# Optimization experiments

Measured on AMD Instinct MI355X. Metric: run time of the kernel, lower is better.

## Reference

```python
import jax, jax.numpy as jnp
import numpy as np
from jax import lax


def setup_inputs() -> dict:
    key = jax.random.key(0)
    k1, k2, k3 = jax.random.split(key, 3)
    B, D_IN, D_OUT, DEPTH = 16384, 768, 768, 11
    n_nodes = 2 ** (DEPTH + 1) - 1  # 4095
    l1 = 1.0 / np.sqrt(D_IN)
    l2 = 1.0 / np.sqrt(n_nodes)
    x = jax.random.normal(k1, (B, D_IN), dtype=jnp.float32)
    w1s = jax.random.uniform(k2, (D_IN * n_nodes, 1), minval=-l1, maxval=l1, dtype=jnp.float32)
    w2s = jax.random.uniform(k3, (n_nodes, D_OUT), minval=-l2, maxval=l2, dtype=jnp.float32)
    return {"x": x, "w1s": w1s, "w2s": w2s, "depth": DEPTH}


def reference(x, w1s, w2s, depth):
    # x: [B, d_in]; w1s: [d_in * n_nodes, 1]; w2s: [n_nodes, d_out]
    B, d_in = x.shape
    n_nodes = w2s.shape[0]
    W1 = w1s.reshape(n_nodes, d_in)  # per-node routing hyperplanes

    def step(nodes, _):
        # logit[b] = <x[b], W1[nodes[b]]>  (the per-sample selected-row dot)
        logits = jnp.einsum('bd,bd->b', x, W1[nodes])
        next_nodes = nodes * 2 + (logits >= 0).astype(nodes.dtype) + 1
        return next_nodes, (nodes, logits)

    init = jnp.zeros((B,), dtype=jnp.int32)
    _, (all_nodes, all_logits) = lax.scan(step, init, None, length=depth + 1)
    all_nodes = all_nodes.T                      # [B, depth+1]
    acts = jax.nn.gelu(all_logits.T, approximate=False)  # torch F.gelu is exact erf
    # out[b] = sum_i acts[b,i] * w2s[all_nodes[b,i]]
    out = jnp.einsum('bk,bko->bo', acts, w2s[all_nodes])
    return out
```

## Files before the change

### kernel.cpp

```cpp
#include <hip/hip_runtime.h>
#include <math.h>


#define FFF_LVLS 12
#define FFF_D 768
#define FFF_ROWF4 192
#define FFF_NODES 4095
#define WAVES_PER_BLOCK 16

typedef unsigned short u16x8 __attribute__((ext_vector_type(8)));
typedef unsigned short u16x4 __attribute__((ext_vector_type(4)));

__device__ __forceinline__ float gelu_exact(float v) {
    return 0.5f * v * (1.0f + erff(v * 0.70710678118654752440f));
}

__device__ __forceinline__ unsigned short f32_to_bf16_rne(float f) {
    unsigned int u = __builtin_bit_cast(unsigned int, f);
    u += 0x7FFFu + ((u >> 16) & 1u);
    return (unsigned short)(u >> 16);
}
__device__ __forceinline__ float bf(unsigned short h) {
    return __builtin_bit_cast(float, (unsigned int)h << 16);
}

template <int CTRL>
__device__ __forceinline__ float dpp_shr_add(float v) {
    const int t = __builtin_amdgcn_update_dpp(
        0, __builtin_bit_cast(int, v), CTRL, 0xf, 0xf, true);
    return v + __builtin_bit_cast(float, t);
}

__device__ __forceinline__ float wave_allsum_f32(float v) {
    v = dpp_shr_add<0x111>(v);
    v = dpp_shr_add<0x112>(v);
    v = dpp_shr_add<0x114>(v);
    v = dpp_shr_add<0x118>(v);
    const int i15 = __builtin_amdgcn_readlane(__builtin_bit_cast(int, v), 15);
    const int i31 = __builtin_amdgcn_readlane(__builtin_bit_cast(int, v), 31);
    const int i47 = __builtin_amdgcn_readlane(__builtin_bit_cast(int, v), 47);
    const int i63 = __builtin_amdgcn_readlane(__builtin_bit_cast(int, v), 63);
    return (__builtin_bit_cast(float, i15) + __builtin_bit_cast(float, i31))
         + (__builtin_bit_cast(float, i47) + __builtin_bit_cast(float, i63));
}

__global__ void __launch_bounds__(1024) fff_convert_kernel(
    const float4* __restrict__ w1, const float4* __restrict__ w2,
    ushort4* __restrict__ o1, ushort4* __restrict__ o2, int nf4)
{
    int i = blockIdx.x * blockDim.x + threadIdx.x;
    if (i < nf4) {
        const float4 v = w1[i];
        ushort4 h;
        h.x = f32_to_bf16_rne(v.x); h.y = f32_to_bf16_rne(v.y);
        h.z = f32_to_bf16_rne(v.z); h.w = f32_to_bf16_rne(v.w);
        o1[i] = h;
    } else if (i < 2 * nf4) {
        const int j = i - nf4;
        const float4 v = w2[j];
        ushort4 h;
        h.x = f32_to_bf16_rne(v.x); h.y = f32_to_bf16_rne(v.y);
        h.z = f32_to_bf16_rne(v.z); h.w = f32_to_bf16_rne(v.w);
        o2[j] = h;
    }
}

__global__ void __launch_bounds__(1024) fff_sparse_kernel_bf16(
    const float* __restrict__ x,
    const float* __restrict__ w1s,
    const unsigned short* __restrict__ w1b,
    const unsigned short* __restrict__ w2b,
    float* __restrict__ out,
    int B)
{
    const int wave = threadIdx.x >> 6;
    const int lane = threadIdx.x & 63;
    const int b = blockIdx.x * WAVES_PER_BLOCK + wave;
    if (b >= B) return;

    const float4* __restrict__ xf4 = (const float4*)(x) + (size_t)b * FFF_ROWF4;

    const float4 xA0 = xf4[2 * lane];
    const float4 xA1 = xf4[2 * lane + 1];
    const float4 xB  = xf4[128 + lane];

    float acts[FFF_LVLS];
    int bits = 0;
    int node = 0;

#pragma unroll
    for (int lvl = 0; lvl < FFF_LVLS; ++lvl) {
        const unsigned short* __restrict__ row = w1b + (size_t)node * FFF_D;
        const u16x8 hA = ((const u16x8*)row)[lane];
        const u16x4 hB = ((const u16x4*)(row + 512))[lane];

        float q0 = xA0.x * bf(hA[0]);
        float q1 = xA0.y * bf(hA[1]);
        q0 = fmaf(xA0.z, bf(hA[2]), q0);
        q1 = fmaf(xA0.w, bf(hA[3]), q1);
        q0 = fmaf(xA1.x, bf(hA[4]), q0);
        q1 = fmaf(xA1.y, bf(hA[5]), q1);
        q0 = fmaf(xA1.z, bf(hA[6]), q0);
        q1 = fmaf(xA1.w, bf(hA[7]), q1);
        q0 = fmaf(xB.x,  bf(hB[0]), q0);
        q1 = fmaf(xB.y,  bf(hB[1]), q1);
        q0 = fmaf(xB.z,  bf(hB[2]), q0);
        q1 = fmaf(xB.w,  bf(hB[3]), q1);

        float p = wave_allsum_f32(q0 + q1);

        if (__builtin_expect(fabsf(p) < 0.03f, 0)) {
            const float4* __restrict__ rf = (const float4*)w1s
                                          + (size_t)node * FFF_ROWF4;
            const float4 a0 = rf[2 * lane];
            const float4 a1 = rf[2 * lane + 1];
            const float4 a2 = rf[128 + lane];
            double d0 = (double)xA0.x * (double)a0.x;
            double d1 = (double)xA0.y * (double)a0.y;
            d0 += (double)xA0.z * (double)a0.z;
            d1 += (double)xA0.w * (double)a0.w;
            d0 += (double)xA1.x * (double)a1.x;
            d1 += (double)xA1.y * (double)a1.y;
            d0 += (double)xA1.z * (double)a1.z;
            d1 += (double)xA1.w * (double)a1.w;
            d0 += (double)xB.x  * (double)a2.x;
            d1 += (double)xB.y  * (double)a2.y;
            d0 += (double)xB.z  * (double)a2.z;
            d1 += (double)xB.w  * (double)a2.w;
            double pd = d0 + d1;
#pragma unroll
            for (int m = 32; m > 0; m >>= 1) pd += __shfl_xor(pd, m, 64);
            p = (float)pd;
        }

        acts[lvl] = gelu_exact(p);
        const int s = (p >= 0.0f) ? 1 : 0;
        bits |= s << lvl;
        node = 2 * node + 1 + s;
    }

    float4 accA0 = make_float4(0.f, 0.f, 0.f, 0.f);
    float4 accA1 = make_float4(0.f, 0.f, 0.f, 0.f);
    float4 accB  = make_float4(0.f, 0.f, 0.f, 0.f);

    node = 0;
#pragma unroll
    for (int lvl = 0; lvl < FFF_LVLS; ++lvl) {
        const unsigned short* __restrict__ row = w2b + (size_t)node * FFF_D;
        const u16x8 hA = ((const u16x8*)row)[lane];
        const u16x4 hB = ((const u16x4*)(row + 512))[lane];
        const float a = acts[lvl];
        accA0.x = fmaf(a, bf(hA[0]), accA0.x);
        accA0.y = fmaf(a, bf(hA[1]), accA0.y);
        accA0.z = fmaf(a, bf(hA[2]), accA0.z);
        accA0.w = fmaf(a, bf(hA[3]), accA0.w);
        accA1.x = fmaf(a, bf(hA[4]), accA1.x);
        accA1.y = fmaf(a, bf(hA[5]), accA1.y);
        accA1.z = fmaf(a, bf(hA[6]), accA1.z);
        accA1.w = fmaf(a, bf(hA[7]), accA1.w);
        accB.x  = fmaf(a, bf(hB[0]), accB.x);
        accB.y  = fmaf(a, bf(hB[1]), accB.y);
        accB.z  = fmaf(a, bf(hB[2]), accB.z);
        accB.w  = fmaf(a, bf(hB[3]), accB.w);
        node = 2 * node + 1 + ((bits >> lvl) & 1);
    }

    float4* __restrict__ of4 = (float4*)(out) + (size_t)b * FFF_ROWF4;
    of4[2 * lane]     = accA0;
    of4[2 * lane + 1] = accA1;
    of4[128 + lane]   = accB;
}

__global__ void __launch_bounds__(1024) fff_sparse_kernel_f32(
    const float* __restrict__ x,
    const float* __restrict__ w1s,
    const float* __restrict__ w2s,
    float* __restrict__ out,
    int B)
{
    const int wave = threadIdx.x >> 6;
    const int lane = threadIdx.x & 63;
    const int b = blockIdx.x * WAVES_PER_BLOCK + wave;
    if (b >= B) return;

    const float4* __restrict__ xf4  = (const float4*)x;
    const float4* __restrict__ w1f4 = (const float4*)w1s;
    const float4* __restrict__ w2f4 = (const float4*)w2s;

    const int xb = b * FFF_ROWF4 + lane;
    const float4 xv0 = xf4[xb];
    const float4 xv1 = xf4[xb + 64];
    const float4 xv2 = xf4[xb + 128];

    float acts[FFF_LVLS];
    int bits = 0;
    int node = 0;

#pragma unroll
    for (int lvl = 0; lvl < FFF_LVLS; ++lvl) {
        const int r = node * FFF_ROWF4 + lane;
        const float4 a0 = w1f4[r];
        const float4 a1 = w1f4[r + 64];
        const float4 a2 = w1f4[r + 128];
        float q0 = xv0.x * a0.x;
        float q1 = xv0.y * a0.y;
        q0 = fmaf(xv0.z, a0.z, q0);
        q1 = fmaf(xv0.w, a0.w, q1);
        q0 = fmaf(xv1.x, a1.x, q0);
        q1 = fmaf(xv1.y, a1.y, q1);
        q0 = fmaf(xv1.z, a1.z, q0);
        q1 = fmaf(xv1.w, a1.w, q1);
        q0 = fmaf(xv2.x, a2.x, q0);
        q1 = fmaf(xv2.y, a2.y, q1);
        q0 = fmaf(xv2.z, a2.z, q0);
        q1 = fmaf(xv2.w, a2.w, q1);
        float p = wave_allsum_f32(q0 + q1);
        if (__builtin_expect(fabsf(p) < 1e-4f, 0)) {
            double d0 = (double)xv0.x * (double)a0.x;
            double d1 = (double)xv0.y * (double)a0.y;
            d0 += (double)xv0.z * (double)a0.z;
            d1 += (double)xv0.w * (double)a0.w;
            d0 += (double)xv1.x * (double)a1.x;
            d1 += (double)xv1.y * (double)a1.y;
            d0 += (double)xv1.z * (double)a1.z;
            d1 += (double)xv1.w * (double)a1.w;
            d0 += (double)xv2.x * (double)a2.x;
            d1 += (double)xv2.y * (double)a2.y;
            d0 += (double)xv2.z * (double)a2.z;
            d1 += (double)xv2.w * (double)a2.w;
            double pd = d0 + d1;
#pragma unroll
            for (int m = 32; m > 0; m >>= 1) pd += __shfl_xor(pd, m, 64);
            p = (float)pd;
        }
        acts[lvl] = gelu_exact(p);
        const int s = (p >= 0.0f) ? 1 : 0;
        bits |= s << lvl;
        node = 2 * node + 1 + s;
    }

    float4 acc0 = make_float4(0.f, 0.f, 0.f, 0.f);
    float4 acc1 = make_float4(0.f, 0.f, 0.f, 0.f);
    float4 acc2 = make_float4(0.f, 0.f, 0.f, 0.f);
    node = 0;
#pragma unroll
    for (int lvl = 0; lvl < FFF_LVLS; ++lvl) {
        const int r = node * FFF_ROWF4 + lane;
        const float4 c0 = w2f4[r];
        const float4 c1 = w2f4[r + 64];
        const float4 c2 = w2f4[r + 128];
        const float a = acts[lvl];
        acc0.x = fmaf(a, c0.x, acc0.x); acc0.y = fmaf(a, c0.y, acc0.y);
        acc0.z = fmaf(a, c0.z, acc0.z); acc0.w = fmaf(a, c0.w, acc0.w);
        acc1.x = fmaf(a, c1.x, acc1.x); acc1.y = fmaf(a, c1.y, acc1.y);
        acc1.z = fmaf(a, c1.z, acc1.z); acc1.w = fmaf(a, c1.w, acc1.w);
        acc2.x = fmaf(a, c2.x, acc2.x); acc2.y = fmaf(a, c2.y, acc2.y);
        acc2.z = fmaf(a, c2.z, acc2.z); acc2.w = fmaf(a, c2.w, acc2.w);
        node = 2 * node + 1 + ((bits >> lvl) & 1);
    }

    float4* __restrict__ of4 = (float4*)out;
    const int ob = b * FFF_ROWF4 + lane;
    of4[ob]       = acc0;
    of4[ob + 64]  = acc1;
    of4[ob + 128] = acc2;
}

extern "C" void kernel_launch(void* const* d_in, const int* in_sizes, int n_in,
                              void* d_out, int out_size, void* d_ws, size_t ws_size,
                              hipStream_t stream) {
    const float* x   = (const float*)d_in[0];
    const float* w1s = (const float*)d_in[1];
    const float* w2s = (const float*)d_in[2];
    float* out = (float*)d_out;

    const int B = out_size / FFF_D;
    const int blocks = (B + WAVES_PER_BLOCK - 1) / WAVES_PER_BLOCK;

    const size_t n_elems = (size_t)FFF_NODES * FFF_D;
    const size_t needed = 2 * n_elems * sizeof(unsigned short);

    if (ws_size >= needed) {
        unsigned short* w1b = (unsigned short*)d_ws;
        unsigned short* w2b = w1b + n_elems;
        const int nf4 = (int)(n_elems / 4);
        const int cblocks = (2 * nf4 + 1023) / 1024;
        fff_convert_kernel<<<cblocks, 1024, 0, stream>>>(
            (const float4*)w1s, (const float4*)w2s,
            (ushort4*)w1b, (ushort4*)w2b, nf4);
        fff_sparse_kernel_bf16<<<blocks, WAVES_PER_BLOCK * 64, 0, stream>>>(
            x, w1s, w1b, w2b, out, B);
    } else {
        fff_sparse_kernel_f32<<<blocks, WAVES_PER_BLOCK * 64, 0, stream>>>(
            x, w1s, w2s, out, B);
    }
}
```

Before: 66.40 us.

## Fuse routing and output accumulation into one loop with overlapped row loads

Merges the tree-routing loop and the output accumulation loop into a single pass. At each level the W2 row for the current node and the W1 row for the next node are both issued right after the branch decision, so the W2 gather and GELU/FMA work overlap the latency of the next W1 load. This removes the stored acts/bits and the second serial chain of dependent loads, at the cost of more live registers in the unrolled loop.

```diff
diff --git a/kernel.cpp b/kernel.cpp
--- a/kernel.cpp
+++ b/kernel.cpp
@@ -84,28 +84,29 @@
     const float4 xA1 = xf4[2 * lane + 1];
     const float4 xB  = xf4[128 + lane];
 
-    float acts[FFF_LVLS];
-    int bits = 0;
+    float4 accA0 = make_float4(0.f, 0.f, 0.f, 0.f);
+    float4 accA1 = make_float4(0.f, 0.f, 0.f, 0.f);
+    float4 accB  = make_float4(0.f, 0.f, 0.f, 0.f);
+
     int node = 0;
 
+    u16x8 wA = ((const u16x8*)w1b)[lane];
+    u16x4 wB = ((const u16x4*)(w1b + 512))[lane];
+
 #pragma unroll
     for (int lvl = 0; lvl < FFF_LVLS; ++lvl) {
-        const unsigned short* __restrict__ row = w1b + (size_t)node * FFF_D;
-        const u16x8 hA = ((const u16x8*)row)[lane];
-        const u16x4 hB = ((const u16x4*)(row + 512))[lane];
-
-        float q0 = xA0.x * bf(hA[0]);
-        float q1 = xA0.y * bf(hA[1]);
-        q0 = fmaf(xA0.z, bf(hA[2]), q0);
-        q1 = fmaf(xA0.w, bf(hA[3]), q1);
-        q0 = fmaf(xA1.x, bf(hA[4]), q0);
-        q1 = fmaf(xA1.y, bf(hA[5]), q1);
-        q0 = fmaf(xA1.z, bf(hA[6]), q0);
-        q1 = fmaf(xA1.w, bf(hA[7]), q1);
-        q0 = fmaf(xB.x,  bf(hB[0]), q0);
-        q1 = fmaf(xB.y,  bf(hB[1]), q1);
-        q0 = fmaf(xB.z,  bf(hB[2]), q0);
-        q1 = fmaf(xB.w,  bf(hB[3]), q1);
+        float q0 = xA0.x * bf(wA[0]);
+        float q1 = xA0.y * bf(wA[1]);
+        q0 = fmaf(xA0.z, bf(wA[2]), q0);
+        q1 = fmaf(xA0.w, bf(wA[3]), q1);
+        q0 = fmaf(xA1.x, bf(wA[4]), q0);
+        q1 = fmaf(xA1.y, bf(wA[5]), q1);
+        q0 = fmaf(xA1.z, bf(wA[6]), q0);
+        q1 = fmaf(xA1.w, bf(wA[7]), q1);
+        q0 = fmaf(xB.x,  bf(wB[0]), q0);
+        q1 = fmaf(xB.y,  bf(wB[1]), q1);
+        q0 = fmaf(xB.z,  bf(wB[2]), q0);
+        q1 = fmaf(xB.w,  bf(wB[3]), q1);
 
         float p = wave_allsum_f32(q0 + q1);
 
@@ -133,36 +134,33 @@
             p = (float)pd;
         }
 
-        acts[lvl] = gelu_exact(p);
         const int s = (p >= 0.0f) ? 1 : 0;
-        bits |= s << lvl;
+        const int cur = node;
         node = 2 * node + 1 + s;
-    }
-
-    float4 accA0 = make_float4(0.f, 0.f, 0.f, 0.f);
-    float4 accA1 = make_float4(0.f, 0.f, 0.f, 0.f);
-    float4 accB  = make_float4(0.f, 0.f, 0.f, 0.f);
-
-    node = 0;
-#pragma unroll
-    for (int lvl = 0; lvl < FFF_LVLS; ++lvl) {
-        const unsigned short* __restrict__ row = w2b + (size_t)node * FFF_D;
-        const u16x8 hA = ((const u16x8*)row)[lane];
-        const u16x4 hB = ((const u16x4*)(row + 512))[lane];
-        const float a = acts[lvl];
-        accA0.x = fmaf(a, bf(hA[0]), accA0.x);
-        accA0.y = fmaf(a, bf(hA[1]), accA0.y);
-        accA0.z = fmaf(a, bf(hA[2]), accA0.z);
-        accA0.w = fmaf(a, bf(hA[3]), accA0.w);
-        accA1.x = fmaf(a, bf(hA[4]), accA1.x);
-        accA1.y = fmaf(a, bf(hA[5]), accA1.y);
-        accA1.z = fmaf(a, bf(hA[6]), accA1.z);
-        accA1.w = fmaf(a, bf(hA[7]), accA1.w);
-        accB.x  = fmaf(a, bf(hB[0]), accB.x);
-        accB.y  = fmaf(a, bf(hB[1]), accB.y);
-        accB.z  = fmaf(a, bf(hB[2]), accB.z);
-        accB.w  = fmaf(a, bf(hB[3]), accB.w);
-        node = 2 * node + 1 + ((bits >> lvl) & 1);
+
+        const unsigned short* __restrict__ row2 = w2b + (size_t)cur * FFF_D;
+        const u16x8 cA = ((const u16x8*)row2)[lane];
+        const u16x4 cB = ((const u16x4*)(row2 + 512))[lane];
+
+        if (lvl + 1 < FFF_LVLS) {
+            const unsigned short* __restrict__ row1 = w1b + (size_t)node * FFF_D;
+            wA = ((const u16x8*)row1)[lane];
+            wB = ((const u16x4*)(row1 + 512))[lane];
+        }
+
+        const float a = gelu_exact(p);
+        accA0.x = fmaf(a, bf(cA[0]), accA0.x);
+        accA0.y = fmaf(a, bf(cA[1]), accA0.y);
+        accA0.z = fmaf(a, bf(cA[2]), accA0.z);
+        accA0.w = fmaf(a, bf(cA[3]), accA0.w);
+        accA1.x = fmaf(a, bf(cA[4]), accA1.x);
+        accA1.y = fmaf(a, bf(cA[5]), accA1.y);
+        accA1.z = fmaf(a, bf(cA[6]), accA1.z);
+        accA1.w = fmaf(a, bf(cA[7]), accA1.w);
+        accB.x  = fmaf(a, bf(cB[0]), accB.x);
+        accB.y  = fmaf(a, bf(cB[1]), accB.y);
+        accB.z  = fmaf(a, bf(cB[2]), accB.z);
+        accB.w  = fmaf(a, bf(cB[3]), accB.w);
     }
 
     float4* __restrict__ of4 = (float4*)(out) + (size_t)b * FFF_ROWF4;
```

New measurement: 85.11 us. +28.2%, slower.

## Switch weights to fp16 with dot2 and stage top tree levels in LDS

Applied to the files above, without the earlier changes.

Weights are now converted to fp16 instead of bf16, and the routing dot products use packed fp16 dot2 instructions on fp16-converted x. Each block also preloads the first 31 W1 rows and 15 W2 rows into shared memory (about 70 KB) so the shallow tree levels read from LDS instead of global/L2. The fp32 fallback threshold is narrowed from 0.03 to 0.01. The large LDS allocation limits blocks per CU, and every block pays to reload it. Rounding x to fp16 may also flip more routing decisions than the narrower fallback catches.

```diff
diff --git a/kernel.cpp b/kernel.cpp
--- a/kernel.cpp
+++ b/kernel.cpp
@@ -7,21 +7,23 @@
 #define FFF_ROWF4 192
 #define FFF_NODES 4095
 #define WAVES_PER_BLOCK 16
-
-typedef unsigned short u16x8 __attribute__((ext_vector_type(8)));
-typedef unsigned short u16x4 __attribute__((ext_vector_type(4)));
+#define NTOP_W1 31
+#define NTOP_W2 15
+
+typedef _Float16 f16x8 __attribute__((ext_vector_type(8)));
+typedef _Float16 f16x4 __attribute__((ext_vector_type(4)));
+typedef _Float16 f16x2 __attribute__((ext_vector_type(2)));
 
 __device__ __forceinline__ float gelu_exact(float v) {
     return 0.5f * v * (1.0f + erff(v * 0.70710678118654752440f));
 }
 
-__device__ __forceinline__ unsigned short f32_to_bf16_rne(float f) {
-    unsigned int u = __builtin_bit_cast(unsigned int, f);
-    u += 0x7FFFu + ((u >> 16) & 1u);
-    return (unsigned short)(u >> 16);
-}
-__device__ __forceinline__ float bf(unsigned short h) {
-    return __builtin_bit_cast(float, (unsigned int)h << 16);
+__device__ __forceinline__ float fdot2(f16x2 a, f16x2 b, float c) {
+#if __has_builtin(__builtin_amdgcn_fdot2)
+    return __builtin_amdgcn_fdot2(a, b, c, false);
+#else
+    return c + (float)a.x * (float)b.x + (float)a.y * (float)b.y;
+#endif
 }
 
 template <int CTRL>
@@ -46,70 +48,95 @@
 
 __global__ void __launch_bounds__(1024) fff_convert_kernel(
     const float4* __restrict__ w1, const float4* __restrict__ w2,
-    ushort4* __restrict__ o1, ushort4* __restrict__ o2, int nf4)
+    f16x4* __restrict__ o1, f16x4* __restrict__ o2, int nf4)
 {
     int i = blockIdx.x * blockDim.x + threadIdx.x;
     if (i < nf4) {
         const float4 v = w1[i];
-        ushort4 h;
-        h.x = f32_to_bf16_rne(v.x); h.y = f32_to_bf16_rne(v.y);
-        h.z = f32_to_bf16_rne(v.z); h.w = f32_to_bf16_rne(v.w);
+        f16x4 h;
+        h.x = (_Float16)v.x; h.y = (_Float16)v.y;
+        h.z = (_Float16)v.z; h.w = (_Float16)v.w;
         o1[i] = h;
     } else if (i < 2 * nf4) {
         const int j = i - nf4;
         const float4 v = w2[j];
-        ushort4 h;
-        h.x = f32_to_bf16_rne(v.x); h.y = f32_to_bf16_rne(v.y);
-        h.z = f32_to_bf16_rne(v.z); h.w = f32_to_bf16_rne(v.w);
+        f16x4 h;
+        h.x = (_Float16)v.x; h.y = (_Float16)v.y;
+        h.z = (_Float16)v.z; h.w = (_Float16)v.w;
         o2[j] = h;
     }
 }
 
-__global__ void __launch_bounds__(1024) fff_sparse_kernel_bf16(
+__global__ void __launch_bounds__(1024) fff_sparse_kernel_f16(
     const float* __restrict__ x,
     const float* __restrict__ w1s,
-    const unsigned short* __restrict__ w1b,
-    const unsigned short* __restrict__ w2b,
+    const _Float16* __restrict__ w1h,
+    const _Float16* __restrict__ w2h,
     float* __restrict__ out,
     int B)
 {
+    __shared__ _Float16 lds_w[(NTOP_W1 + NTOP_W2) * FFF_D];
+
+    {
+        uint4* __restrict__ ldsv = (uint4*)lds_w;
+        const uint4* __restrict__ s1 = (const uint4*)w1h;
+        const uint4* __restrict__ s2 = (const uint4*)w2h;
+        const int n1 = NTOP_W1 * FFF_D / 8;
+        const int nt = (NTOP_W1 + NTOP_W2) * FFF_D / 8;
+        for (int i = threadIdx.x; i < nt; i += 1024)
+            ldsv[i] = (i < n1) ? s1[i] : s2[i - n1];
+    }
+    __syncthreads();
+
     const int wave = threadIdx.x >> 6;
     const int lane = threadIdx.x & 63;
     const int b = blockIdx.x * WAVES_PER_BLOCK + wave;
     if (b >= B) return;
 
+    const _Float16* __restrict__ lds_w1 = lds_w;
+    const _Float16* __restrict__ lds_w2 = lds_w + NTOP_W1 * FFF_D;
+
     const float4* __restrict__ xf4 = (const float4*)(x) + (size_t)b * FFF_ROWF4;
 
     const float4 xA0 = xf4[2 * lane];
     const float4 xA1 = xf4[2 * lane + 1];
     const float4 xB  = xf4[128 + lane];
 
+    f16x2 xh0 = {(_Float16)xA0.x, (_Float16)xA0.y};
+    f16x2 xh1 = {(_Float16)xA0.z, (_Float16)xA0.w};
+    f16x2 xh2 = {(_Float16)xA1.x, (_Float16)xA1.y};
+    f16x2 xh3 = {(_Float16)xA1.z, (_Float16)xA1.w};
+    f16x2 xh4 = {(_Float16)xB.x,  (_Float16)xB.y};
+    f16x2 xh5 = {(_Float16)xB.z,  (_Float16)xB.w};
+
     float acts[FFF_LVLS];
     int bits = 0;
     int node = 0;
 
 #pragma unroll
     for (int lvl = 0; lvl < FFF_LVLS; ++lvl) {
-        const unsigned short* __restrict__ row = w1b + (size_t)node * FFF_D;
-        const u16x8 hA = ((const u16x8*)row)[lane];
-        const u16x4 hB = ((const u16x4*)(row + 512))[lane];
-
-        float q0 = xA0.x * bf(hA[0]);
-        float q1 = xA0.y * bf(hA[1]);
-        q0 = fmaf(xA0.z, bf(hA[2]), q0);
-        q1 = fmaf(xA0.w, bf(hA[3]), q1);
-        q0 = fmaf(xA1.x, bf(hA[4]), q0);
-        q1 = fmaf(xA1.y, bf(hA[5]), q1);
-        q0 = fmaf(xA1.z, bf(hA[6]), q0);
-        q1 = fmaf(xA1.w, bf(hA[7]), q1);
-        q0 = fmaf(xB.x,  bf(hB[0]), q0);
-        q1 = fmaf(xB.y,  bf(hB[1]), q1);
-        q0 = fmaf(xB.z,  bf(hB[2]), q0);
-        q1 = fmaf(xB.w,  bf(hB[3]), q1);
+        f16x8 hA;
+        f16x4 hB;
+        if (lvl <= 4) {
+            const _Float16* row = lds_w1 + node * FFF_D;
+            hA = ((const f16x8*)row)[lane];
+            hB = ((const f16x4*)(row + 512))[lane];
+        } else {
+            const _Float16* row = w1h + (size_t)node * FFF_D;
+            hA = ((const f16x8*)row)[lane];
+            hB = ((const f16x4*)(row + 512))[lane];
+        }
+
+        float q0 = fdot2(xh0, f16x2{hA[0], hA[1]}, 0.f);
+        float q1 = fdot2(xh1, f16x2{hA[2], hA[3]}, 0.f);
+        q0 = fdot2(xh2, f16x2{hA[4], hA[5]}, q0);
+        q1 = fdot2(xh3, f16x2{hA[6], hA[7]}, q1);
+        q0 = fdot2(xh4, f16x2{hB[0], hB[1]}, q0);
+        q1 = fdot2(xh5, f16x2{hB[2], hB[3]}, q1);
 
         float p = wave_allsum_f32(q0 + q1);
 
-        if (__builtin_expect(fabsf(p) < 0.03f, 0)) {
+        if (__builtin_expect(fabsf(p) < 0.01f, 0)) {
             const float4* __restrict__ rf = (const float4*)w1s
                                           + (size_t)node * FFF_ROWF4;
             const float4 a0 = rf[2 * lane];
@@ -146,22 +173,30 @@
     node = 0;
 #pragma unroll
     for (int lvl = 0; lvl < FFF_LVLS; ++lvl) {
-        const unsigned short* __restrict__ row = w2b + (size_t)node * FFF_D;
-        const u16x8 hA = ((const u16x8*)row)[lane];
-        const u16x4 hB = ((const u16x4*)(row + 512))[lane];
+        f16x8 hA;
+        f16x4 hB;
+        if (lvl <= 3) {
+            const _Float16* row = lds_w2 + node * FFF_D;
+            hA = ((const f16x8*)row)[lane];
+            hB = ((const f16x4*)(row + 512))[lane];
+        } else {
+            const _Float16* row = w2h + (size_t)node * FFF_D;
+            hA = ((const f16x8*)row)[lane];
+            hB = ((const f16x4*)(row + 512))[lane];
+        }
         const float a = acts[lvl];
-        accA0.x = fmaf(a, bf(hA[0]), accA0.x);
-        accA0.y = fmaf(a, bf(hA[1]), accA0.y);
-        accA0.z = fmaf(a, bf(hA[2]), accA0.z);
-        accA0.w = fmaf(a, bf(hA[3]), accA0.w);
-        accA1.x = fmaf(a, bf(hA[4]), accA1.x);
-        accA1.y = fmaf(a, bf(hA[5]), accA1.y);
-        accA1.z = fmaf(a, bf(hA[6]), accA1.z);
-        accA1.w = fmaf(a, bf(hA[7]), accA1.w);
-        accB.x  = fmaf(a, bf(hB[0]), accB.x);
-        accB.y  = fmaf(a, bf(hB[1]), accB.y);
-        accB.z  = fmaf(a, bf(hB[2]), accB.z);
-        accB.w  = fmaf(a, bf(hB[3]), accB.w);
+        accA0.x = fmaf(a, (float)hA[0], accA0.x);
+        accA0.y = fmaf(a, (float)hA[1], accA0.y);
+        accA0.z = fmaf(a, (float)hA[2], accA0.z);
+        accA0.w = fmaf(a, (float)hA[3], accA0.w);
+        accA1.x = fmaf(a, (float)hA[4], accA1.x);
+        accA1.y = fmaf(a, (float)hA[5], accA1.y);
+        accA1.z = fmaf(a, (float)hA[6], accA1.z);
+        accA1.w = fmaf(a, (float)hA[7], accA1.w);
+        accB.x  = fmaf(a, (float)hB[0], accB.x);
+        accB.y  = fmaf(a, (float)hB[1], accB.y);
+        accB.z  = fmaf(a, (float)hB[2], accB.z);
+        accB.w  = fmaf(a, (float)hB[3], accB.w);
         node = 2 * node + 1 + ((bits >> lvl) & 1);
     }
 
@@ -170,6 +205,9 @@
     of4[2 * lane + 1] = accA1;
     of4[128 + lane]   = accB;
 }
+
+template <int CTRL>
+__device__ __forceinline__ float dpp_shr_add_f(float v);
 
 __global__ void __launch_bounds__(1024) fff_sparse_kernel_f32(
     const float* __restrict__ x,
@@ -278,18 +316,18 @@
     const int blocks = (B + WAVES_PER_BLOCK - 1) / WAVES_PER_BLOCK;
 
     const size_t n_elems = (size_t)FFF_NODES * FFF_D;
-    const size_t needed = 2 * n_elems * sizeof(unsigned short);
+    const size_t needed = 2 * n_elems * sizeof(_Float16);
 
     if (ws_size >= needed) {
-        unsigned short* w1b = (unsigned short*)d_ws;
-        unsigned short* w2b = w1b + n_elems;
+        _Float16* w1h = (_Float16*)d_ws;
+        _Float16* w2h = w1h + n_elems;
         const int nf4 = (int)(n_elems / 4);
         const int cblocks = (2 * nf4 + 1023) / 1024;
         fff_convert_kernel<<<cblocks, 1024, 0, stream>>>(
             (const float4*)w1s, (const float4*)w2s,
-            (ushort4*)w1b, (ushort4*)w2b, nf4);
-        fff_sparse_kernel_bf16<<<blocks, WAVES_PER_BLOCK * 64, 0, stream>>>(
-            x, w1s, w1b, w2b, out, B);
+            (f16x4*)w1h, (f16x4*)w2h, nf4);
+        fff_sparse_kernel_f16<<<blocks, WAVES_PER_BLOCK * 64, 0, stream>>>(
+            x, w1s, w1h, w2h, out, B);
     } else {
         fff_sparse_kernel_f32<<<blocks, WAVES_PER_BLOCK * 64, 0, stream>>>(
             x, w1s, w2s, out, B);
```

Result: faster. 63.08 us (-5.0%).
